# Kernel tuning notes

Hardware: AMD Instinct MI355X
Metric: run time of the kernel (lower is better)

Reference implementation:

```python
import jax, jax.numpy as jnp
import numpy as np

N_SLOTS = 524288
DIM_MEM = 128
DIM_IN = 1024
SHIFT_RADIUS = 3
EPS = 1e-8  # torch cosine_similarity eps


def setup_inputs() -> dict:
    key = jax.random.key(0)
    k1, k2, k3, k4, k5 = jax.random.split(key, 5)
    n_factors = DIM_MEM + 1 + 1 + (2 * SHIFT_RADIUS + 1) + 1  # 138
    return {
        "input_from_controller": jax.random.normal(k1, (DIM_IN,), dtype=jnp.float32),
        "previous_weighting": jax.random.uniform(k2, (N_SLOTS,), dtype=jnp.float32),
        "memory": jax.random.normal(k3, (N_SLOTS, DIM_MEM), dtype=jnp.float32),
        "W_wf": jax.random.normal(k4, (DIM_IN, n_factors), dtype=jnp.float32) * 0.02,
        "b_wf": jax.random.normal(k5, (n_factors,), dtype=jnp.float32) * 0.02,
    }


def _get_weighting(input_from_controller, previous_weighting, memory, W_wf, b_wf):
    factors = input_from_controller @ W_wf + b_wf  # [138]
    M = DIM_MEM
    key_v = factors[:M]                       # [M]
    key_s = factors[M]                        # scalar (beta)
    gate = jax.nn.softmax(factors[M + 1:M + 2])      # size-1 softmax -> 1.0 (faithful)
    shift_w = jax.nn.softmax(factors[M + 2:M + 2 + 2 * SHIFT_RADIUS + 1])  # [2r+1]
    sharpening = jax.nn.relu(factors[-1]) + 1.0

    # content addressing: cosine similarity of each memory row with key_v
    mem_norm = jnp.maximum(jnp.linalg.norm(memory, axis=1), EPS)  # [N]
    key_norm = jnp.maximum(jnp.linalg.norm(key_v), EPS)
    content_w = (memory @ key_v) / (mem_norm * key_norm)          # [N]
    content_w = jax.nn.softmax(key_s * content_w)

    gated_w = content_w * gate[0] + (1.0 - gate[0]) * previous_weighting

    # circular convolution: shifted[i] = sum_j gated[(i - r + j) % N] * shift_w[j]
    shifted_w = jnp.zeros_like(gated_w)
    for j in range(2 * SHIFT_RADIUS + 1):  # small fixed tap count (7)
        shifted_w = shifted_w + shift_w[j] * jnp.roll(gated_w, SHIFT_RADIUS - j)

    pw = shifted_w ** sharpening
    return pw / pw.sum()


def reference(input_from_controller, previous_weighting, memory, W_wf, b_wf):
    w = _get_weighting(input_from_controller, previous_weighting, memory, W_wf, b_wf)
    read_vector = w @ memory  # read head forward
    return read_vector
```

## Files before the change

### kernel.cpp

```cpp
#include <hip/hip_runtime.h>
#include <math.h>

#define N_SLOTS 524288
#define DIM_MEM 128
#define DIM_IN 1024
#define NFACT 138
#define EPSF 1e-8f
#define CPB 4
#define ROWS_PC 64
#define NPAIR 70
#define PAD 33


__global__ __launch_bounds__(256) void k_factors(const float* __restrict__ x,
                                                 const float* __restrict__ W,
                                                 const float* __restrict__ b,
                                                 float* __restrict__ factors) {
    int j = threadIdx.x;
    int i0 = blockIdx.x * 32;
    if (j < NFACT) {
        float acc = 0.f;
        #pragma unroll 8
        for (int i = i0; i < i0 + 32; ++i)
            acc = fmaf(x[i], W[(size_t)i * NFACT + j], acc);
        if (blockIdx.x == 0) acc += b[j];
        atomicAdd(&factors[j], acc);
    }
}

__global__ void k_derived(const float* __restrict__ f, float* __restrict__ d) {
    int l = threadIdx.x;
    float v = f[l] * f[l] + f[l + 64] * f[l + 64];
    for (int off = 32; off; off >>= 1) v += __shfl_xor(v, off, 64);
    if (l == 0) {
        float key_norm = fmaxf(sqrtf(v), EPSF);
        d[0] = f[128] / key_norm;
        float m = f[130];
        for (int j = 1; j < 7; ++j) m = fmaxf(m, f[130 + j]);
        float e[7], s = 0.f;
        for (int j = 0; j < 7; ++j) { e[j] = expf(f[130 + j] - m); s += e[j]; }
        for (int j = 0; j < 7; ++j) d[1 + j] = e[j] / s;
        d[8] = fmaxf(f[137], 0.f) + 1.f;
    }
}

__global__ __launch_bounds__(256) void k_main(const float* __restrict__ mem,
                                              const float* __restrict__ keyv,
                                              const float* __restrict__ der,
                                              float* __restrict__ num,
                                              double* __restrict__ P_acc) {
    __shared__ float part[2 * NPAIR * PAD];
    __shared__ float sums[2 * NPAIR];
    __shared__ float e_sh[NPAIR];
    __shared__ float w_sh[ROWS_PC];
    __shared__ float colpart[8][DIM_MEM];
    __shared__ float psum[8];

    const int tid  = threadIdx.x;
    const int lane = tid & 31;
    const int hw   = tid >> 5;
    const float4* mem4 = (const float4*)mem;
    const float4 k4 = ((const float4*)keyv)[lane];
    const float d0 = der[0];
    const float sharp = der[8];
    float sw[7];
    #pragma unroll
    for (int d = 0; d < 7; ++d) sw[d] = der[1 + d];

    float4 acc = make_float4(0.f, 0.f, 0.f, 0.f);
    float wsum = 0.f;

    for (int c = 0; c < CPB; ++c) {
        const int r0 = blockIdx.x * (CPB * ROWS_PC) + c * ROWS_PC;
        const int rbase = r0 + hw * 8;

        float4 row[8];
        #pragma unroll
        for (int j = 0; j < 8; ++j)
            row[j] = mem4[(size_t)(rbase + j) * 32 + lane];
        #pragma unroll
        for (int j = 0; j < 8; ++j) {
            float dp = row[j].x * k4.x + row[j].y * k4.y + row[j].z * k4.z + row[j].w * k4.w;
            float np = row[j].x * row[j].x + row[j].y * row[j].y + row[j].z * row[j].z + row[j].w * row[j].w;
            int p = 3 + hw * 8 + j;
            part[(p * 2 + 0) * PAD + lane] = dp;
            part[(p * 2 + 1) * PAD + lane] = np;
        }
        if (hw < 6) {
            int hr = (hw < 3) ? (r0 - 3 + hw) : (r0 + ROWS_PC + (hw - 3));
            hr &= (N_SLOTS - 1);
            int p = (hw < 3) ? hw : (64 + hw);
            float4 m4 = mem4[(size_t)hr * 32 + lane];
            part[(p * 2 + 0) * PAD + lane] =
                m4.x * k4.x + m4.y * k4.y + m4.z * k4.z + m4.w * k4.w;
            part[(p * 2 + 1) * PAD + lane] =
                m4.x * m4.x + m4.y * m4.y + m4.z * m4.z + m4.w * m4.w;
        }
        __syncthreads();

        if (tid < 2 * NPAIR) {
            float s = 0.f;
            #pragma unroll
            for (int l = 0; l < 32; ++l) s += part[tid * PAD + l];
            sums[tid] = s;
        }
        __syncthreads();

        if (tid < NPAIR) {
            float dot = sums[tid * 2], n2 = sums[tid * 2 + 1];
            e_sh[tid] = __expf(d0 * dot / fmaxf(sqrtf(n2), EPSF));
        }
        __syncthreads();

        if (tid < ROWS_PC) {
            float t = 0.f;
            #pragma unroll
            for (int d = 0; d < 7; ++d) t = fmaf(sw[d], e_sh[tid + d], t);
            w_sh[tid] = __expf(sharp * __logf(t));
        }
        __syncthreads();

        #pragma unroll
        for (int j = 0; j < 8; ++j) {
            float w = w_sh[hw * 8 + j];
            acc.x = fmaf(w, row[j].x, acc.x);
            acc.y = fmaf(w, row[j].y, acc.y);
            acc.z = fmaf(w, row[j].z, acc.z);
            acc.w = fmaf(w, row[j].w, acc.w);
            wsum += w;
        }
        __syncthreads();
    }

    ((float4*)colpart[hw])[lane] = acc;
    if (lane == 0) psum[hw] = wsum;
    __syncthreads();
    if (tid < DIM_MEM) {
        float s = 0.f;
        #pragma unroll
        for (int h = 0; h < 8; ++h) s += colpart[h][tid];
        atomicAdd(&num[tid], s);
    }
    if (tid == 0) {
        float s = 0.f;
        #pragma unroll
        for (int h = 0; h < 8; ++h) s += psum[h];
        atomicAdd(P_acc, (double)s);
    }
}

__global__ void k_final(const float* __restrict__ num,
                        const double* __restrict__ P_acc,
                        float* __restrict__ out) {
    out[threadIdx.x] = num[threadIdx.x] / (float)(*P_acc);
}

extern "C" void kernel_launch(void* const* d_in, const int* in_sizes, int n_in,
                              void* d_out, int out_size, void* d_ws, size_t ws_size,
                              hipStream_t stream) {
    const float* x   = (const float*)d_in[0];
    const float* mem = (const float*)d_in[2];
    const float* W   = (const float*)d_in[3];
    const float* b   = (const float*)d_in[4];
    float* out = (float*)d_out;

    char* ws = (char*)d_ws;
    float*  factors = (float*)ws;
    float*  derived = (float*)(ws + 1024);
    double* P_acc   = (double*)(ws + 2048);
    float*  num     = (float*)(ws + 2176);

    hipMemsetAsync(ws, 0, 4096, stream);

    k_factors<<<DIM_IN / 32, 256, 0, stream>>>(x, W, b, factors);
    k_derived<<<1, 64, 0, stream>>>(factors, derived);
    k_main<<<N_SLOTS / (CPB * ROWS_PC), 256, 0, stream>>>(mem, factors, derived, num, P_acc);
    k_final<<<1, DIM_MEM, 0, stream>>>(num, P_acc, out);
}
```

Baseline: 381.1 us.

## Double-buffer memory row loads, merge reduction stages, replace atomics with per-block partials

The main kernel now prefetches the next chunk's rows and halo into a second register buffer while computing the current chunk, so global loads overlap compute. The dot and norm partials are packed into a single float2 shared array, which merges two sync stages into one, and the trailing barrier is dropped. The global float and double atomics are replaced with per-block partial slots, reduced by a wider final kernel. Double buffering doubles the register footprint for rows and may lower occupancy, and the final kernel now reads every block's partials.

```diff
diff --git a/kernel.cpp b/kernel.cpp
--- a/kernel.cpp
+++ b/kernel.cpp
@@ -9,7 +9,9 @@
 #define CPB 4
 #define ROWS_PC 64
 #define NPAIR 70
-#define PAD 33
+#define PADH 33
+#define NBLK (N_SLOTS / (CPB * ROWS_PC))
+#define PSTRIDE 132
 
 
 __global__ __launch_bounds__(256) void k_factors(const float* __restrict__ x,
@@ -47,10 +49,8 @@
 __global__ __launch_bounds__(256) void k_main(const float* __restrict__ mem,
                                               const float* __restrict__ keyv,
                                               const float* __restrict__ der,
-                                              float* __restrict__ num,
-                                              double* __restrict__ P_acc) {
-    __shared__ float part[2 * NPAIR * PAD];
-    __shared__ float sums[2 * NPAIR];
+                                              float* __restrict__ partials) {
+    __shared__ float2 part2[NPAIR * PADH];
     __shared__ float e_sh[NPAIR];
     __shared__ float w_sh[ROWS_PC];
     __shared__ float colpart[8][DIM_MEM];
@@ -70,45 +70,60 @@
     float4 acc = make_float4(0.f, 0.f, 0.f, 0.f);
     float wsum = 0.f;
 
-    for (int c = 0; c < CPB; ++c) {
-        const int r0 = blockIdx.x * (CPB * ROWS_PC) + c * ROWS_PC;
-        const int rbase = r0 + hw * 8;
-
-        float4 row[8];
+    float4 bufA[8], bufB[8], haloA, haloB;
+    const int base = blockIdx.x * (CPB * ROWS_PC);
+
+    {
+        const int r0 = base, rbase = r0 + hw * 8;
         #pragma unroll
         for (int j = 0; j < 8; ++j)
-            row[j] = mem4[(size_t)(rbase + j) * 32 + lane];
-        #pragma unroll
-        for (int j = 0; j < 8; ++j) {
-            float dp = row[j].x * k4.x + row[j].y * k4.y + row[j].z * k4.z + row[j].w * k4.w;
-            float np = row[j].x * row[j].x + row[j].y * row[j].y + row[j].z * row[j].z + row[j].w * row[j].w;
-            int p = 3 + hw * 8 + j;
-            part[(p * 2 + 0) * PAD + lane] = dp;
-            part[(p * 2 + 1) * PAD + lane] = np;
-        }
+            bufA[j] = mem4[(size_t)(rbase + j) * 32 + lane];
         if (hw < 6) {
             int hr = (hw < 3) ? (r0 - 3 + hw) : (r0 + ROWS_PC + (hw - 3));
             hr &= (N_SLOTS - 1);
+            haloA = mem4[(size_t)hr * 32 + lane];
+        }
+    }
+
+    #pragma unroll
+    for (int c = 0; c < CPB; ++c) {
+        float4* cur   = (c & 1) ? bufB : bufA;
+        float4* nxt   = (c & 1) ? bufA : bufB;
+        float4& curh  = (c & 1) ? haloB : haloA;
+        float4& nxth  = (c & 1) ? haloA : haloB;
+
+        if (c + 1 < CPB) {
+            const int r0 = base + (c + 1) * ROWS_PC, rbase = r0 + hw * 8;
+            #pragma unroll
+            for (int j = 0; j < 8; ++j)
+                nxt[j] = mem4[(size_t)(rbase + j) * 32 + lane];
+            if (hw < 6) {
+                int hr = (hw < 3) ? (r0 - 3 + hw) : (r0 + ROWS_PC + (hw - 3));
+                hr &= (N_SLOTS - 1);
+                nxth = mem4[(size_t)hr * 32 + lane];
+            }
+        }
+
+        #pragma unroll
+        for (int j = 0; j < 8; ++j) {
+            float dp = cur[j].x * k4.x + cur[j].y * k4.y + cur[j].z * k4.z + cur[j].w * k4.w;
+            float np = cur[j].x * cur[j].x + cur[j].y * cur[j].y + cur[j].z * cur[j].z + cur[j].w * cur[j].w;
+            part2[(3 + hw * 8 + j) * PADH + lane] = make_float2(dp, np);
+        }
+        if (hw < 6) {
             int p = (hw < 3) ? hw : (64 + hw);
-            float4 m4 = mem4[(size_t)hr * 32 + lane];
-            part[(p * 2 + 0) * PAD + lane] =
-                m4.x * k4.x + m4.y * k4.y + m4.z * k4.z + m4.w * k4.w;
-            part[(p * 2 + 1) * PAD + lane] =
-                m4.x * m4.x + m4.y * m4.y + m4.z * m4.z + m4.w * m4.w;
+            float dp = curh.x * k4.x + curh.y * k4.y + curh.z * k4.z + curh.w * k4.w;
+            float np = curh.x * curh.x + curh.y * curh.y + curh.z * curh.z + curh.w * curh.w;
+            part2[p * PADH + lane] = make_float2(dp, np);
         }
         __syncthreads();
 
-        if (tid < 2 * NPAIR) {
-            float s = 0.f;
+        if (tid < NPAIR) {
+            const float2* q = &part2[tid * PADH];
+            float d = 0.f, n = 0.f;
             #pragma unroll
-            for (int l = 0; l < 32; ++l) s += part[tid * PAD + l];
-            sums[tid] = s;
-        }
-        __syncthreads();
-
-        if (tid < NPAIR) {
-            float dot = sums[tid * 2], n2 = sums[tid * 2 + 1];
-            e_sh[tid] = __expf(d0 * dot / fmaxf(sqrtf(n2), EPSF));
+            for (int l = 0; l < 32; ++l) { float2 v = q[l]; d += v.x; n += v.y; }
+            e_sh[tid] = __expf(d0 * d / fmaxf(sqrtf(n), EPSF));
         }
         __syncthreads();
 
@@ -123,36 +138,45 @@
         #pragma unroll
         for (int j = 0; j < 8; ++j) {
             float w = w_sh[hw * 8 + j];
-            acc.x = fmaf(w, row[j].x, acc.x);
-            acc.y = fmaf(w, row[j].y, acc.y);
-            acc.z = fmaf(w, row[j].z, acc.z);
-            acc.w = fmaf(w, row[j].w, acc.w);
+            acc.x = fmaf(w, cur[j].x, acc.x);
+            acc.y = fmaf(w, cur[j].y, acc.y);
+            acc.z = fmaf(w, cur[j].z, acc.z);
+            acc.w = fmaf(w, cur[j].w, acc.w);
             wsum += w;
         }
-        __syncthreads();
     }
 
     ((float4*)colpart[hw])[lane] = acc;
     if (lane == 0) psum[hw] = wsum;
     __syncthreads();
+    float* slot = partials + (size_t)blockIdx.x * PSTRIDE;
     if (tid < DIM_MEM) {
         float s = 0.f;
         #pragma unroll
         for (int h = 0; h < 8; ++h) s += colpart[h][tid];
-        atomicAdd(&num[tid], s);
+        slot[tid] = s;
     }
     if (tid == 0) {
         float s = 0.f;
         #pragma unroll
         for (int h = 0; h < 8; ++h) s += psum[h];
-        atomicAdd(P_acc, (double)s);
-    }
-}
-
-__global__ void k_final(const float* __restrict__ num,
-                        const double* __restrict__ P_acc,
+        slot[128] = s;
+    }
+}
+
+__global__ void k_final(const float* __restrict__ partials,
                         float* __restrict__ out) {
-    out[threadIdx.x] = num[threadIdx.x] / (float)(*P_acc);
+    const int c = blockIdx.x, t = threadIdx.x;
+    float s = 0.f, p = 0.f;
+    for (int b = t; b < NBLK; b += 64) {
+        s += partials[(size_t)b * PSTRIDE + c];
+        p += partials[(size_t)b * PSTRIDE + 128];
+    }
+    for (int off = 32; off; off >>= 1) {
+        s += __shfl_xor(s, off, 64);
+        p += __shfl_xor(p, off, 64);
+    }
+    if (t == 0) out[c] = s / p;
 }
 
 extern "C" void kernel_launch(void* const* d_in, const int* in_sizes, int n_in,
@@ -165,15 +189,14 @@
     float* out = (float*)d_out;
 
     char* ws = (char*)d_ws;
-    float*  factors = (float*)ws;
-    float*  derived = (float*)(ws + 1024);
-    double* P_acc   = (double*)(ws + 2048);
-    float*  num     = (float*)(ws + 2176);
+    float* factors  = (float*)ws;
+    float* derived  = (float*)(ws + 1024);
+    float* partials = (float*)(ws + 4096);
 
     hipMemsetAsync(ws, 0, 4096, stream);
 
     k_factors<<<DIM_IN / 32, 256, 0, stream>>>(x, W, b, factors);
     k_derived<<<1, 64, 0, stream>>>(factors, derived);
-    k_main<<<N_SLOTS / (CPB * ROWS_PC), 256, 0, stream>>>(mem, factors, derived, num, P_acc);
-    k_final<<<1, DIM_MEM, 0, stream>>>(num, P_acc, out);
-}
+    k_main<<<NBLK, 256, 0, stream>>>(mem, factors, derived, partials);
+    k_final<<<DIM_MEM, 64, 0, stream>>>(partials, out);
+}
```

New measurement: 385.7 us. Within noise of the previous version (+1.2%).
